# Performance work log

Hardware: AMD Instinct MI355X
Metric: run time of the kernel (lower is better)

## Reference

```python
import jax, jax.numpy as jnp
import numpy as np

N_NODES = 100000
N_EDGES = 3200000
F_IN = 512
HIDDEN = 64
N_CLASSES = 64


def setup_inputs() -> dict:
    key = jax.random.key(0)
    ks = jax.random.split(key, 6)
    node_features = jax.random.normal(ks[0], (N_NODES, F_IN), dtype=jnp.float32)
    edge_rows = jax.random.randint(ks[1], (N_EDGES,), 0, N_NODES, dtype=jnp.int32)
    edge_cols = jax.random.randint(ks[2], (N_EDGES,), 0, N_NODES, dtype=jnp.int32)
    edge_vals = jax.random.uniform(ks[3], (N_EDGES,), dtype=jnp.float32)
    W1 = jax.random.normal(ks[4], (F_IN, HIDDEN), dtype=jnp.float32) / np.sqrt(F_IN)
    b1 = jnp.zeros((HIDDEN,), dtype=jnp.float32)
    W2 = jax.random.normal(ks[5], (HIDDEN, N_CLASSES), dtype=jnp.float32) / np.sqrt(HIDDEN)
    b2 = jnp.zeros((N_CLASSES,), dtype=jnp.float32)
    return {
        "node_features": node_features,
        "edge_rows": edge_rows,
        "edge_cols": edge_cols,
        "edge_vals": edge_vals,
        "W1": W1,
        "b1": b1,
        "W2": W2,
        "b2": b2,
    }


def reference(node_features, edge_rows, edge_cols, edge_vals, W1, b1, W2, b2):
    # MLP node transform (inference: dropout is identity, no norms)
    h = jax.nn.relu(node_features @ W1 + b1)          # [N, HIDDEN]
    logits = h @ W2 + b2                              # [N, C]
    # smoother @ logits : sparse [N,N] COO times dense [N,C]
    messages = edge_vals[:, None] * logits[edge_cols]  # [E, C]
    out = jax.ops.segment_sum(messages, edge_rows, num_segments=N_NODES)
    return out
```

## Files before the change

### kernel.cpp

```cpp
#include <hip/hip_runtime.h>
#include <hip/hip_bf16.h>
#include <stdint.h>

#define N_NODES 100000
#define N_EDGES 3200000
#define F_IN    512
#define HIDDEN  64
#define NCLS    64

#define BROWS   64
#define NBKT    1563
#define CHUNK   4096
#define CAP     2432
#define NCOARSE 25
#define CAP1    135168
#define C2BLKS  33
#define OVF_CAP 8192
#define SENTINEL ((int)0x80000000)
#define NZERO   (NBKT*16 + NCOARSE*16 + 16)

typedef float v4f __attribute__((ext_vector_type(4)));
typedef short v8s __attribute__((ext_vector_type(8)));

__device__ __forceinline__ unsigned short f2bf(float f){
  unsigned u = __float_as_uint(f);
  u += 0x7fffu + ((u >> 16) & 1u);
  return (unsigned short)(u >> 16);
}
__device__ __forceinline__ float bflo(unsigned u){ return __uint_as_float(u << 16); }
__device__ __forceinline__ float bfhi(unsigned u){ return __uint_as_float(u & 0xffff0000u); }

__global__ void prep_weights(const float* __restrict__ W1, const float* __restrict__ W2,
                             unsigned short* __restrict__ w1f, unsigned short* __restrict__ w2f,
                             int* __restrict__ zeroc){
  int t = blockIdx.x * 256 + threadIdx.x;
  if (t < NZERO) zeroc[t] = 0;
  if (t < 16*4*64*8){
    int j = t & 7, lane = (t >> 3) & 63, nt = (t >> 9) & 3, ks = t >> 11;
    int m = lane & 15, q = lane >> 4;
    int k = ks*32 + q*8 + j, n = nt*16 + m;
    w1f[t] = f2bf(W1[k*HIDDEN + n]);
  } else {
    int u = t - 16*4*64*8;
    if (u < 2*4*64*8){
      int j = u & 7, lane = (u >> 3) & 63, nt = (u >> 9) & 3, ks = u >> 11;
      int m = lane & 15, q = lane >> 4;
      int k = ks*32 + q*8 + j, n = nt*16 + m;
      w2f[u] = f2bf(W2[k*NCLS + n]);
    }
  }
}

__global__ __launch_bounds__(256) void mlp_kernel(
    const float* __restrict__ X, const float* __restrict__ b1,
    const float* __restrict__ b2,
    const unsigned short* __restrict__ w1f, const unsigned short* __restrict__ w2f,
    unsigned short* __restrict__ logits){
  __shared__ __align__(16) float lds[4][16][68];
  int tid  = threadIdx.x;
  int wid  = tid >> 6, lane = tid & 63;
  int m    = lane & 15, q = lane >> 4;
  int base = blockIdx.x * 64 + wid * 16;
  if (base > N_NODES - 16) base = N_NODES - 16;

  const float* rp = X + (size_t)(base + m) * F_IN + q * 8;
  const v8s* w1v = (const v8s*)w1f;
  const v8s* w2v = (const v8s*)w2f;

  v4f a0c = {0,0,0,0}, a1c = {0,0,0,0}, a2c = {0,0,0,0}, a3c = {0,0,0,0};
  #pragma unroll
  for (int ks = 0; ks < 16; ++ks){
    const float4* pa = (const float4*)(rp + ks * 32);
    float4 x0 = pa[0], x1 = pa[1];
    v8s af;
    af[0]=(short)f2bf(x0.x); af[1]=(short)f2bf(x0.y); af[2]=(short)f2bf(x0.z); af[3]=(short)f2bf(x0.w);
    af[4]=(short)f2bf(x1.x); af[5]=(short)f2bf(x1.y); af[6]=(short)f2bf(x1.z); af[7]=(short)f2bf(x1.w);
    a0c = __builtin_amdgcn_mfma_f32_16x16x32_bf16(af, w1v[(ks*4+0)*64 + lane], a0c, 0,0,0);
    a1c = __builtin_amdgcn_mfma_f32_16x16x32_bf16(af, w1v[(ks*4+1)*64 + lane], a1c, 0,0,0);
    a2c = __builtin_amdgcn_mfma_f32_16x16x32_bf16(af, w1v[(ks*4+2)*64 + lane], a2c, 0,0,0);
    a3c = __builtin_amdgcn_mfma_f32_16x16x32_bf16(af, w1v[(ks*4+3)*64 + lane], a3c, 0,0,0);
  }

  float b1v0 = b1[m], b1v1 = b1[16+m], b1v2 = b1[32+m], b1v3 = b1[48+m];
  #pragma unroll
  for (int r = 0; r < 4; ++r){
    int row = q*4 + r;
    lds[wid][row][     m] = fmaxf(a0c[r] + b1v0, 0.f);
    lds[wid][row][16 + m] = fmaxf(a1c[r] + b1v1, 0.f);
    lds[wid][row][32 + m] = fmaxf(a2c[r] + b1v2, 0.f);
    lds[wid][row][48 + m] = fmaxf(a3c[r] + b1v3, 0.f);
  }
  __syncthreads();

  v4f c0 = {0,0,0,0}, c1 = {0,0,0,0}, c2 = {0,0,0,0}, c3 = {0,0,0,0};
  #pragma unroll
  for (int k2 = 0; k2 < 2; ++k2){
    const float4* ph = (const float4*)&lds[wid][m][k2*32 + q*8];
    float4 h0 = ph[0], h1 = ph[1];
    v8s af;
    af[0]=(short)f2bf(h0.x); af[1]=(short)f2bf(h0.y); af[2]=(short)f2bf(h0.z); af[3]=(short)f2bf(h0.w);
    af[4]=(short)f2bf(h1.x); af[5]=(short)f2bf(h1.y); af[6]=(short)f2bf(h1.z); af[7]=(short)f2bf(h1.w);
    c0 = __builtin_amdgcn_mfma_f32_16x16x32_bf16(af, w2v[(k2*4+0)*64 + lane], c0, 0,0,0);
    c1 = __builtin_amdgcn_mfma_f32_16x16x32_bf16(af, w2v[(k2*4+1)*64 + lane], c1, 0,0,0);
    c2 = __builtin_amdgcn_mfma_f32_16x16x32_bf16(af, w2v[(k2*4+2)*64 + lane], c2, 0,0,0);
    c3 = __builtin_amdgcn_mfma_f32_16x16x32_bf16(af, w2v[(k2*4+3)*64 + lane], c3, 0,0,0);
  }

  float b2v0 = b2[m], b2v1 = b2[16+m], b2v2 = b2[32+m], b2v3 = b2[48+m];
  unsigned short* lp = logits + (size_t)base * NCLS;
  #pragma unroll
  for (int r = 0; r < 4; ++r){
    int row = q*4 + r;
    lp[row*NCLS +      m] = f2bf(c0[r] + b2v0);
    lp[row*NCLS + 16 + m] = f2bf(c1[r] + b2v1);
    lp[row*NCLS + 32 + m] = f2bf(c2[r] + b2v2);
    lp[row*NCLS + 48 + m] = f2bf(c3[r] + b2v3);
  }
}

__global__ __launch_bounds__(256) void scat1(
    const int* __restrict__ rows, const int* __restrict__ cols,
    const float* __restrict__ vals, int* __restrict__ c1cur,
    int* __restrict__ ovf_cnt, int4* __restrict__ ovf,
    int2* __restrict__ ebkt1){
  __shared__ int  lcnt[32];
  __shared__ int  lbase[32];
  __shared__ int2 stage[CHUNK];
  __shared__ int  sdst[CHUNK];
  int t = threadIdx.x;
  int base = blockIdx.x * CHUNK;
  int cnt  = min(CHUNK, N_EDGES - base);

  if (t < 32) lcnt[t] = 0;
  __syncthreads();

  int r[16];
  #pragma unroll
  for (int k = 0; k < 16; ++k){
    int li = t + k*256;
    if (li < cnt){
      r[k] = rows[base + li];
      atomicAdd(&lcnt[r[k] >> 12], 1);
    } else r[k] = -1;
  }
  __syncthreads();

  if (t < 32){
    int cme = lcnt[t];
    int v = cme;
    #pragma unroll
    for (int o = 1; o < 32; o <<= 1){
      int u = __shfl_up(v, o);
      if (t >= o) v += u;
    }
    int excl = v - cme;
    if (cme){
      int g = atomicAdd(&c1cur[t*16], cme);
      lbase[t] = t*CAP1 + g - excl;
    }
    lcnt[t] = excl;
  }
  __syncthreads();

  #pragma unroll
  for (int k = 0; k < 16; ++k){
    if (r[k] >= 0){
      int li = t + k*256;
      int c  = cols[base + li];
      float vv = vals[base + li];
      int b  = r[k] >> 12;
      int pos = atomicAdd(&lcnt[b], 1);
      int dest = lbase[b] + pos;
      if (dest < b*CAP1 + CAP1){
        stage[pos] = make_int2(((r[k] & 4095) << 17) | c, __float_as_int(vv));
        sdst[pos]  = lbase[b];
      } else {
        sdst[pos] = SENTINEL;
        int o = atomicAdd(ovf_cnt, 1);
        if (o < OVF_CAP) ovf[o] = make_int4(r[k], c, __float_as_int(vv), 0);
      }
    }
  }
  __syncthreads();

  for (int j = t; j < cnt; j += 256){
    int d = sdst[j];
    if (d != SENTINEL) ebkt1[d + j] = stage[j];
  }
}

__global__ __launch_bounds__(256) void scat2(
    const int* __restrict__ c1cur, const int2* __restrict__ ebkt1,
    int* __restrict__ bcur, int* __restrict__ ovf_cnt, int4* __restrict__ ovf,
    int2* __restrict__ ebkt){
  __shared__ int  lcnt[64];
  __shared__ int  lbase[64];
  __shared__ int2 stage[CHUNK];
  __shared__ int  sdst[CHUNK];
  int t = threadIdx.x;
  int c = blockIdx.x / C2BLKS;
  int k0 = blockIdx.x % C2BLKS;

  int cntc = c1cur[c*16];
  if (cntc > CAP1) cntc = CAP1;
  int start = k0 * CHUNK;
  if (start >= cntc) return;
  int cnt = min(CHUNK, cntc - start);
  const int2* src = ebkt1 + (size_t)c * CAP1 + start;

  if (t < 64) lcnt[t] = 0;
  __syncthreads();

  int2 ev[16];
  #pragma unroll
  for (int k = 0; k < 16; ++k){
    int li = t + k*256;
    if (li < cnt){
      ev[k] = src[li];
      atomicAdd(&lcnt[(((unsigned)ev[k].x) >> 17) >> 6], 1);
    } else ev[k].x = -1;
  }
  __syncthreads();

  if (t < 64){
    int cme = lcnt[t];
    int v = cme;
    #pragma unroll
    for (int o = 1; o < 64; o <<= 1){
      int u = __shfl_up(v, o);
      if (t >= o) v += u;
    }
    int excl = v - cme;
    if (cme){
      int gb = c*64 + t;
      int g = atomicAdd(&bcur[gb*16], cme);
      lbase[t] = gb*CAP + g - excl;
    }
    lcnt[t] = excl;
  }
  __syncthreads();

  #pragma unroll
  for (int k = 0; k < 16; ++k){
    if (ev[k].x >= 0){
      unsigned x = (unsigned)ev[k].x;
      int lr12 = (int)(x >> 17);
      int fb   = lr12 >> 6;
      int pos = atomicAdd(&lcnt[fb], 1);
      int dest = lbase[fb] + pos;
      if (dest < (c*64 + fb)*CAP + CAP){
        stage[pos] = make_int2(((lr12 & 63) << 17) | (int)(x & 0x1FFFFu), ev[k].y);
        sdst[pos]  = lbase[fb];
      } else {
        sdst[pos] = SENTINEL;
        int o = atomicAdd(ovf_cnt, 1);
        if (o < OVF_CAP) ovf[o] = make_int4(c*4096 + lr12, (int)(x & 0x1FFFFu), ev[k].y, 0);
      }
    }
  }
  __syncthreads();

  for (int j = t; j < cnt; j += 256){
    int d = sdst[j];
    if (d != SENTINEL) ebkt[d + j] = stage[j];
  }
}

__global__ __launch_bounds__(256) void bucket_agg(
    const int* __restrict__ bcur, const int2* __restrict__ ebkt,
    const unsigned short* __restrict__ logits, float* __restrict__ out){
  __shared__ int2 sorted[CAP];
  __shared__ int  rc[BROWS];
  __shared__ int  rbase[BROWS + 1];
  __shared__ int  rcur[BROWS];
  int b = blockIdx.x, t = threadIdx.x;
  int w = t >> 6, lane = t & 63;
  int h = lane & 15, sel = lane >> 4;

  if (t < BROWS) rc[t] = 0;
  __syncthreads();

  int cnt = bcur[b * 16];
  if (cnt > CAP) cnt = CAP;
  const int2* ep = ebkt + (size_t)b * CAP;

  for (int j = t; j < cnt; j += 256){
    int x = ((const int*)ep)[2*j];
    atomicAdd(&rc[((unsigned)x) >> 17], 1);
  }
  __syncthreads();

  if (t < BROWS){
    int c = rc[t];
    int v = c;
    #pragma unroll
    for (int o = 1; o < 64; o <<= 1){
      int u = __shfl_up(v, o);
      if (lane >= o) v += u;
    }
    rbase[t + 1] = v;
    rcur[t]      = v - c;
    if (t == 0) rbase[0] = 0;
  }
  __syncthreads();

  for (int j = t; j < cnt; j += 256){
    int2 ev = ep[j];
    int pos = atomicAdd(&rcur[((unsigned)ev.x) >> 17], 1);
    sorted[pos] = ev;
  }
  __syncthreads();

  const uint2* lg = (const uint2*)logits;
  int row0 = b * BROWS;
  for (int n = w; n < BROWS; n += 4){
    int node = row0 + n;
    if (node >= N_NODES) break;
    int s = rbase[n], e = rbase[n + 1];
    float a0 = 0.f, a1 = 0.f, a2 = 0.f, a3 = 0.f;
    int i = s;
    for (; i + 16 <= e; i += 16){
      int2 e0 = sorted[i      + sel];
      int2 e1 = sorted[i + 4  + sel];
      int2 e2 = sorted[i + 8  + sel];
      int2 e3 = sorted[i + 12 + sel];
      uint2 u0 = lg[((size_t)(e0.x & 0x1FFFF) << 4) + h];
      uint2 u1 = lg[((size_t)(e1.x & 0x1FFFF) << 4) + h];
      uint2 u2 = lg[((size_t)(e2.x & 0x1FFFF) << 4) + h];
      uint2 u3 = lg[((size_t)(e3.x & 0x1FFFF) << 4) + h];
      float v0 = __int_as_float(e0.y), v1 = __int_as_float(e1.y);
      float v2 = __int_as_float(e2.y), v3 = __int_as_float(e3.y);
      a0 = fmaf(v0, bflo(u0.x), a0); a1 = fmaf(v0, bfhi(u0.x), a1);
      a2 = fmaf(v0, bflo(u0.y), a2); a3 = fmaf(v0, bfhi(u0.y), a3);
      a0 = fmaf(v1, bflo(u1.x), a0); a1 = fmaf(v1, bfhi(u1.x), a1);
      a2 = fmaf(v1, bflo(u1.y), a2); a3 = fmaf(v1, bfhi(u1.y), a3);
      a0 = fmaf(v2, bflo(u2.x), a0); a1 = fmaf(v2, bfhi(u2.x), a1);
      a2 = fmaf(v2, bflo(u2.y), a2); a3 = fmaf(v2, bfhi(u2.y), a3);
      a0 = fmaf(v3, bflo(u3.x), a0); a1 = fmaf(v3, bfhi(u3.x), a1);
      a2 = fmaf(v3, bflo(u3.y), a2); a3 = fmaf(v3, bfhi(u3.y), a3);
    }
    for (; i < e; i += 4){
      int idx = i + sel;
      int col = 0; float v = 0.f;
      if (idx < e){ int2 evv = sorted[idx]; col = evv.x & 0x1FFFF; v = __int_as_float(evv.y); }
      uint2 u = lg[((size_t)col << 4) + h];
      a0 = fmaf(v, bflo(u.x), a0); a1 = fmaf(v, bfhi(u.x), a1);
      a2 = fmaf(v, bflo(u.y), a2); a3 = fmaf(v, bfhi(u.y), a3);
    }
    a0 += __shfl_xor(a0, 16); a0 += __shfl_xor(a0, 32);
    a1 += __shfl_xor(a1, 16); a1 += __shfl_xor(a1, 32);
    a2 += __shfl_xor(a2, 16); a2 += __shfl_xor(a2, 32);
    a3 += __shfl_xor(a3, 16); a3 += __shfl_xor(a3, 32);
    if (sel == 0){
      float4* op = (float4*)(out + (size_t)node * NCLS);
      op[h] = make_float4(a0, a1, a2, a3);
    }
  }
}

__global__ __launch_bounds__(256) void ovf_apply(
    const int* __restrict__ ovf_cnt, const int4* __restrict__ ovf,
    const unsigned short* __restrict__ logits, float* __restrict__ out){
  int cnt = ovf_cnt[0];
  if (cnt > OVF_CAP) cnt = OVF_CAP;
  long total = (long)cnt * 64;
  for (long i = (long)blockIdx.x * 256 + threadIdx.x; i < total; i += (long)gridDim.x * 256){
    int e = (int)(i >> 6), c = (int)(i & 63);
    int4 ev = ovf[e];
    float lv = bflo(logits[((size_t)ev.y << 6) + c]);
    atomicAdd(&out[((size_t)ev.x << 6) + c], __int_as_float(ev.z) * lv);
  }
}

__global__ void scatter_atomic(const int* __restrict__ rows, const int* __restrict__ cols,
                               const float* __restrict__ vals,
                               const unsigned short* __restrict__ logits,
                               float* __restrict__ out){
  long g = (long)blockIdx.x * 256 + threadIdx.x;
  int e = (int)(g >> 6), c = (int)(g & 63);
  if (e < N_EDGES){
    float lv = __uint_as_float(((unsigned)logits[(size_t)cols[e] * NCLS + c]) << 16);
    atomicAdd(&out[(size_t)rows[e] * NCLS + c], vals[e] * lv);
  }
}

extern "C" void kernel_launch(void* const* d_in, const int* in_sizes, int n_in,
                              void* d_out, int out_size, void* d_ws, size_t ws_size,
                              hipStream_t stream){
  const float* X     = (const float*)d_in[0];
  const int*   erows = (const int*)  d_in[1];
  const int*   ecols = (const int*)  d_in[2];
  const float* evals = (const float*)d_in[3];
  const float* W1    = (const float*)d_in[4];
  const float* b1    = (const float*)d_in[5];
  const float* W2    = (const float*)d_in[6];
  const float* b2    = (const float*)d_in[7];
  float* out = (float*)d_out;

  char* ws = (char*)d_ws;
  size_t off = 0;
  auto alloc = [&](size_t bytes) -> char* {
    char* p = ws + off;
    off = (off + bytes + 255) & ~(size_t)255;
    return p;
  };
  unsigned short* logits = (unsigned short*)alloc((size_t)N_NODES * NCLS * 2);
  unsigned short* w1f    = (unsigned short*)alloc(16*4*64*8 * 2);
  unsigned short* w2f    = (unsigned short*)alloc(2*4*64*8 * 2);
  int*  bcur  = (int*)alloc((size_t)NZERO * 4);
  int*  c1cur = bcur + NBKT*16;
  int*  ovfc  = bcur + NBKT*16 + NCOARSE*16;
  int4* ovf   = (int4*)alloc((size_t)OVF_CAP * 16);
  int2* ebkt1 = (int2*)alloc((size_t)NCOARSE * CAP1 * 8);
  int2* ebkt  = (int2*)alloc((size_t)NBKT * CAP * 8);
  size_t full_need = off;

  prep_weights<<<144, 256, 0, stream>>>(W1, W2, w1f, w2f, bcur);
  mlp_kernel<<<(N_NODES + 63) / 64, 256, 0, stream>>>(X, b1, b2, w1f, w2f, logits);

  if (ws_size >= full_need){
    scat1<<<(N_EDGES + CHUNK - 1) / CHUNK, 256, 0, stream>>>(
        erows, ecols, evals, c1cur, ovfc, ovf, ebkt1);
    scat2<<<NCOARSE * C2BLKS, 256, 0, stream>>>(
        c1cur, ebkt1, bcur, ovfc, ovf, ebkt);
    bucket_agg<<<NBKT, 256, 0, stream>>>(bcur, ebkt, logits, out);
    ovf_apply<<<256, 256, 0, stream>>>(ovfc, ovf, logits, out);
  } else {
    hipMemsetAsync(out, 0, (size_t)N_NODES * NCLS * 4, stream);
    scatter_atomic<<<(int)(((long)N_EDGES * 64 + 255) / 256), 256, 0, stream>>>(
        erows, ecols, evals, logits, out);
  }
}
```

Baseline: 451.0 us.

## Co-schedule weight prep with edge scatter and MLP with second scatter pass

```diff
diff --git a/kernel.cpp b/kernel.cpp
--- a/kernel.cpp
+++ b/kernel.cpp
@@ -11,13 +11,19 @@
 #define BROWS   64
 #define NBKT    1563
 #define CHUNK   4096
+#define CHUNK2  2048
 #define CAP     2432
 #define NCOARSE 25
 #define CAP1    135168
-#define C2BLKS  33
+#define C2BLKS  66
 #define OVF_CAP 8192
 #define SENTINEL ((int)0x80000000)
 #define NZERO   (NBKT*16 + NCOARSE*16 + 16)
+
+#define PREP_BLKS 144
+#define SC1_BLKS  782
+#define MLP_BLKS  1563
+#define SC2_BLKS  (NCOARSE * C2BLKS)
 
 typedef float v4f __attribute__((ext_vector_type(4)));
 typedef short v8s __attribute__((ext_vector_type(8)));
@@ -30,105 +36,39 @@
 __device__ __forceinline__ float bflo(unsigned u){ return __uint_as_float(u << 16); }
 __device__ __forceinline__ float bfhi(unsigned u){ return __uint_as_float(u & 0xffff0000u); }
 
-__global__ void prep_weights(const float* __restrict__ W1, const float* __restrict__ W2,
-                             unsigned short* __restrict__ w1f, unsigned short* __restrict__ w2f,
-                             int* __restrict__ zeroc){
-  int t = blockIdx.x * 256 + threadIdx.x;
-  if (t < NZERO) zeroc[t] = 0;
-  if (t < 16*4*64*8){
-    int j = t & 7, lane = (t >> 3) & 63, nt = (t >> 9) & 3, ks = t >> 11;
-    int m = lane & 15, q = lane >> 4;
-    int k = ks*32 + q*8 + j, n = nt*16 + m;
-    w1f[t] = f2bf(W1[k*HIDDEN + n]);
-  } else {
-    int u = t - 16*4*64*8;
-    if (u < 2*4*64*8){
-      int j = u & 7, lane = (u >> 3) & 63, nt = (u >> 9) & 3, ks = u >> 11;
-      int m = lane & 15, q = lane >> 4;
-      int k = ks*32 + q*8 + j, n = nt*16 + m;
-      w2f[u] = f2bf(W2[k*NCLS + n]);
-    }
-  }
-}
-
-__global__ __launch_bounds__(256) void mlp_kernel(
-    const float* __restrict__ X, const float* __restrict__ b1,
-    const float* __restrict__ b2,
-    const unsigned short* __restrict__ w1f, const unsigned short* __restrict__ w2f,
-    unsigned short* __restrict__ logits){
-  __shared__ __align__(16) float lds[4][16][68];
-  int tid  = threadIdx.x;
-  int wid  = tid >> 6, lane = tid & 63;
-  int m    = lane & 15, q = lane >> 4;
-  int base = blockIdx.x * 64 + wid * 16;
-  if (base > N_NODES - 16) base = N_NODES - 16;
-
-  const float* rp = X + (size_t)(base + m) * F_IN + q * 8;
-  const v8s* w1v = (const v8s*)w1f;
-  const v8s* w2v = (const v8s*)w2f;
-
-  v4f a0c = {0,0,0,0}, a1c = {0,0,0,0}, a2c = {0,0,0,0}, a3c = {0,0,0,0};
-  #pragma unroll
-  for (int ks = 0; ks < 16; ++ks){
-    const float4* pa = (const float4*)(rp + ks * 32);
-    float4 x0 = pa[0], x1 = pa[1];
-    v8s af;
-    af[0]=(short)f2bf(x0.x); af[1]=(short)f2bf(x0.y); af[2]=(short)f2bf(x0.z); af[3]=(short)f2bf(x0.w);
-    af[4]=(short)f2bf(x1.x); af[5]=(short)f2bf(x1.y); af[6]=(short)f2bf(x1.z); af[7]=(short)f2bf(x1.w);
-    a0c = __builtin_amdgcn_mfma_f32_16x16x32_bf16(af, w1v[(ks*4+0)*64 + lane], a0c, 0,0,0);
-    a1c = __builtin_amdgcn_mfma_f32_16x16x32_bf16(af, w1v[(ks*4+1)*64 + lane], a1c, 0,0,0);
-    a2c = __builtin_amdgcn_mfma_f32_16x16x32_bf16(af, w1v[(ks*4+2)*64 + lane], a2c, 0,0,0);
-    a3c = __builtin_amdgcn_mfma_f32_16x16x32_bf16(af, w1v[(ks*4+3)*64 + lane], a3c, 0,0,0);
-  }
-
-  float b1v0 = b1[m], b1v1 = b1[16+m], b1v2 = b1[32+m], b1v3 = b1[48+m];
-  #pragma unroll
-  for (int r = 0; r < 4; ++r){
-    int row = q*4 + r;
-    lds[wid][row][     m] = fmaxf(a0c[r] + b1v0, 0.f);
-    lds[wid][row][16 + m] = fmaxf(a1c[r] + b1v1, 0.f);
-    lds[wid][row][32 + m] = fmaxf(a2c[r] + b1v2, 0.f);
-    lds[wid][row][48 + m] = fmaxf(a3c[r] + b1v3, 0.f);
-  }
-  __syncthreads();
-
-  v4f c0 = {0,0,0,0}, c1 = {0,0,0,0}, c2 = {0,0,0,0}, c3 = {0,0,0,0};
-  #pragma unroll
-  for (int k2 = 0; k2 < 2; ++k2){
-    const float4* ph = (const float4*)&lds[wid][m][k2*32 + q*8];
-    float4 h0 = ph[0], h1 = ph[1];
-    v8s af;
-    af[0]=(short)f2bf(h0.x); af[1]=(short)f2bf(h0.y); af[2]=(short)f2bf(h0.z); af[3]=(short)f2bf(h0.w);
-    af[4]=(short)f2bf(h1.x); af[5]=(short)f2bf(h1.y); af[6]=(short)f2bf(h1.z); af[7]=(short)f2bf(h1.w);
-    c0 = __builtin_amdgcn_mfma_f32_16x16x32_bf16(af, w2v[(k2*4+0)*64 + lane], c0, 0,0,0);
-    c1 = __builtin_amdgcn_mfma_f32_16x16x32_bf16(af, w2v[(k2*4+1)*64 + lane], c1, 0,0,0);
-    c2 = __builtin_amdgcn_mfma_f32_16x16x32_bf16(af, w2v[(k2*4+2)*64 + lane], c2, 0,0,0);
-    c3 = __builtin_amdgcn_mfma_f32_16x16x32_bf16(af, w2v[(k2*4+3)*64 + lane], c3, 0,0,0);
-  }
-
-  float b2v0 = b2[m], b2v1 = b2[16+m], b2v2 = b2[32+m], b2v3 = b2[48+m];
-  unsigned short* lp = logits + (size_t)base * NCLS;
-  #pragma unroll
-  for (int r = 0; r < 4; ++r){
-    int row = q*4 + r;
-    lp[row*NCLS +      m] = f2bf(c0[r] + b2v0);
-    lp[row*NCLS + 16 + m] = f2bf(c1[r] + b2v1);
-    lp[row*NCLS + 32 + m] = f2bf(c2[r] + b2v2);
-    lp[row*NCLS + 48 + m] = f2bf(c3[r] + b2v3);
-  }
-}
-
-__global__ __launch_bounds__(256) void scat1(
+__global__ __launch_bounds__(256) void k1(
     const int* __restrict__ rows, const int* __restrict__ cols,
     const float* __restrict__ vals, int* __restrict__ c1cur,
     int* __restrict__ ovf_cnt, int4* __restrict__ ovf,
-    int2* __restrict__ ebkt1){
+    int2* __restrict__ ebkt1,
+    const float* __restrict__ W1, const float* __restrict__ W2,
+    unsigned short* __restrict__ w1f, unsigned short* __restrict__ w2f){
   __shared__ int  lcnt[32];
   __shared__ int  lbase[32];
   __shared__ int2 stage[CHUNK];
   __shared__ int  sdst[CHUNK];
   int t = threadIdx.x;
-  int base = blockIdx.x * CHUNK;
+
+  if (blockIdx.x < PREP_BLKS){
+    int g = blockIdx.x * 256 + t;
+    if (g < 16*4*64*8){
+      int j = g & 7, lane = (g >> 3) & 63, nt = (g >> 9) & 3, ks = g >> 11;
+      int m = lane & 15, q = lane >> 4;
+      int k = ks*32 + q*8 + j, n = nt*16 + m;
+      w1f[g] = f2bf(W1[k*HIDDEN + n]);
+    } else {
+      int u = g - 16*4*64*8;
+      if (u < 2*4*64*8){
+        int j = u & 7, lane = (u >> 3) & 63, nt = (u >> 9) & 3, ks = u >> 11;
+        int m = lane & 15, q = lane >> 4;
+        int k = ks*32 + q*8 + j, n = nt*16 + m;
+        w2f[u] = f2bf(W2[k*NCLS + n]);
+      }
+    }
+    return;
+  }
+
+  int base = (blockIdx.x - PREP_BLKS) * CHUNK;
   int cnt  = min(CHUNK, N_EDGES - base);
 
   if (t < 32) lcnt[t] = 0;
@@ -189,32 +129,102 @@
   }
 }
 
-__global__ __launch_bounds__(256) void scat2(
+__global__ __launch_bounds__(256) void k2(
+    const float* __restrict__ X, const float* __restrict__ b1,
+    const float* __restrict__ b2,
+    const unsigned short* __restrict__ w1f, const unsigned short* __restrict__ w2f,
+    unsigned short* __restrict__ logits,
     const int* __restrict__ c1cur, const int2* __restrict__ ebkt1,
     int* __restrict__ bcur, int* __restrict__ ovf_cnt, int4* __restrict__ ovf,
     int2* __restrict__ ebkt){
-  __shared__ int  lcnt[64];
-  __shared__ int  lbase[64];
-  __shared__ int2 stage[CHUNK];
-  __shared__ int  sdst[CHUNK];
-  int t = threadIdx.x;
-  int c = blockIdx.x / C2BLKS;
-  int k0 = blockIdx.x % C2BLKS;
+  __shared__ __align__(16) char smem[25088];
+  int tid = threadIdx.x;
+
+  if (blockIdx.x < MLP_BLKS){
+    float (*lds)[16][68] = (float (*)[16][68])smem;
+    int wid  = tid >> 6, lane = tid & 63;
+    int m    = lane & 15, q = lane >> 4;
+    int base = blockIdx.x * 64 + wid * 16;
+    if (base > N_NODES - 16) base = N_NODES - 16;
+
+    const float* rp = X + (size_t)(base + m) * F_IN + q * 8;
+    const v8s* w1v = (const v8s*)w1f;
+    const v8s* w2v = (const v8s*)w2f;
+
+    v4f a0c = {0,0,0,0}, a1c = {0,0,0,0}, a2c = {0,0,0,0}, a3c = {0,0,0,0};
+    #pragma unroll
+    for (int ks = 0; ks < 16; ++ks){
+      const float4* pa = (const float4*)(rp + ks * 32);
+      float4 x0 = pa[0], x1 = pa[1];
+      v8s af;
+      af[0]=(short)f2bf(x0.x); af[1]=(short)f2bf(x0.y); af[2]=(short)f2bf(x0.z); af[3]=(short)f2bf(x0.w);
+      af[4]=(short)f2bf(x1.x); af[5]=(short)f2bf(x1.y); af[6]=(short)f2bf(x1.z); af[7]=(short)f2bf(x1.w);
+      a0c = __builtin_amdgcn_mfma_f32_16x16x32_bf16(af, w1v[(ks*4+0)*64 + lane], a0c, 0,0,0);
+      a1c = __builtin_amdgcn_mfma_f32_16x16x32_bf16(af, w1v[(ks*4+1)*64 + lane], a1c, 0,0,0);
+      a2c = __builtin_amdgcn_mfma_f32_16x16x32_bf16(af, w1v[(ks*4+2)*64 + lane], a2c, 0,0,0);
+      a3c = __builtin_amdgcn_mfma_f32_16x16x32_bf16(af, w1v[(ks*4+3)*64 + lane], a3c, 0,0,0);
+    }
+
+    float b1v0 = b1[m], b1v1 = b1[16+m], b1v2 = b1[32+m], b1v3 = b1[48+m];
+    #pragma unroll
+    for (int r = 0; r < 4; ++r){
+      int row = q*4 + r;
+      lds[wid][row][     m] = fmaxf(a0c[r] + b1v0, 0.f);
+      lds[wid][row][16 + m] = fmaxf(a1c[r] + b1v1, 0.f);
+      lds[wid][row][32 + m] = fmaxf(a2c[r] + b1v2, 0.f);
+      lds[wid][row][48 + m] = fmaxf(a3c[r] + b1v3, 0.f);
+    }
+    __syncthreads();
+
+    v4f c0 = {0,0,0,0}, c1 = {0,0,0,0}, c2 = {0,0,0,0}, c3 = {0,0,0,0};
+    #pragma unroll
+    for (int k2i = 0; k2i < 2; ++k2i){
+      const float4* ph = (const float4*)&lds[wid][m][k2i*32 + q*8];
+      float4 h0 = ph[0], h1 = ph[1];
+      v8s af;
+      af[0]=(short)f2bf(h0.x); af[1]=(short)f2bf(h0.y); af[2]=(short)f2bf(h0.z); af[3]=(short)f2bf(h0.w);
+      af[4]=(short)f2bf(h1.x); af[5]=(short)f2bf(h1.y); af[6]=(short)f2bf(h1.z); af[7]=(short)f2bf(h1.w);
+      c0 = __builtin_amdgcn_mfma_f32_16x16x32_bf16(af, w2v[(k2i*4+0)*64 + lane], c0, 0,0,0);
+      c1 = __builtin_amdgcn_mfma_f32_16x16x32_bf16(af, w2v[(k2i*4+1)*64 + lane], c1, 0,0,0);
+      c2 = __builtin_amdgcn_mfma_f32_16x16x32_bf16(af, w2v[(k2i*4+2)*64 + lane], c2, 0,0,0);
+      c3 = __builtin_amdgcn_mfma_f32_16x16x32_bf16(af, w2v[(k2i*4+3)*64 + lane], c3, 0,0,0);
+    }
+
+    float b2v0 = b2[m], b2v1 = b2[16+m], b2v2 = b2[32+m], b2v3 = b2[48+m];
+    unsigned short* lp = logits + (size_t)base * NCLS;
+    #pragma unroll
+    for (int r = 0; r < 4; ++r){
+      int row = q*4 + r;
+      lp[row*NCLS +      m] = f2bf(c0[r] + b2v0);
+      lp[row*NCLS + 16 + m] = f2bf(c1[r] + b2v1);
+      lp[row*NCLS + 32 + m] = f2bf(c2[r] + b2v2);
+      lp[row*NCLS + 48 + m] = f2bf(c3[r] + b2v3);
+    }
+    return;
+  }
+
+  int2* stage = (int2*)smem;
+  int*  sdst  = (int*)(smem + 16384);
+  int*  lcnt  = (int*)(smem + 24576);
+  int*  lbase = (int*)(smem + 24832);
+  int sbid = blockIdx.x - MLP_BLKS;
+  int c  = sbid / C2BLKS;
+  int k0 = sbid % C2BLKS;
 
   int cntc = c1cur[c*16];
   if (cntc > CAP1) cntc = CAP1;
-  int start = k0 * CHUNK;
+  int start = k0 * CHUNK2;
   if (start >= cntc) return;
-  int cnt = min(CHUNK, cntc - start);
+  int cnt = min(CHUNK2, cntc - start);
   const int2* src = ebkt1 + (size_t)c * CAP1 + start;
 
-  if (t < 64) lcnt[t] = 0;
-  __syncthreads();
-
-  int2 ev[16];
+  if (tid < 64) lcnt[tid] = 0;
+  __syncthreads();
+
+  int2 ev[8];
   #pragma unroll
-  for (int k = 0; k < 16; ++k){
-    int li = t + k*256;
+  for (int k = 0; k < 8; ++k){
+    int li = tid + k*256;
     if (li < cnt){
       ev[k] = src[li];
       atomicAdd(&lcnt[(((unsigned)ev[k].x) >> 17) >> 6], 1);
@@ -222,26 +232,26 @@
   }
   __syncthreads();
 
-  if (t < 64){
-    int cme = lcnt[t];
+  if (tid < 64){
+    int cme = lcnt[tid];
     int v = cme;
     #pragma unroll
     for (int o = 1; o < 64; o <<= 1){
       int u = __shfl_up(v, o);
-      if (t >= o) v += u;
+      if (tid >= o) v += u;
     }
     int excl = v - cme;
     if (cme){
-      int gb = c*64 + t;
+      int gb = c*64 + tid;
       int g = atomicAdd(&bcur[gb*16], cme);
-      lbase[t] = gb*CAP + g - excl;
-    }
-    lcnt[t] = excl;
+      lbase[tid] = gb*CAP + g - excl;
+    }
+    lcnt[tid] = excl;
   }
   __syncthreads();
 
   #pragma unroll
-  for (int k = 0; k < 16; ++k){
+  for (int k = 0; k < 8; ++k){
     if (ev[k].x >= 0){
       unsigned x = (unsigned)ev[k].x;
       int lr12 = (int)(x >> 17);
@@ -260,7 +270,7 @@
   }
   __syncthreads();
 
-  for (int j = t; j < cnt; j += 256){
+  for (int j = tid; j < cnt; j += 256){
     int d = sdst[j];
     if (d != SENTINEL) ebkt[d + j] = stage[j];
   }
@@ -268,7 +278,8 @@
 
 __global__ __launch_bounds__(256) void bucket_agg(
     const int* __restrict__ bcur, const int2* __restrict__ ebkt,
-    const unsigned short* __restrict__ logits, float* __restrict__ out){
+    const unsigned short* __restrict__ logits, float* __restrict__ out,
+    const int* __restrict__ ovf_cnt, const int4* __restrict__ ovfl){
   __shared__ int2 sorted[CAP];
   __shared__ int  rc[BROWS];
   __shared__ int  rbase[BROWS + 1];
@@ -283,6 +294,8 @@
   int cnt = bcur[b * 16];
   if (cnt > CAP) cnt = CAP;
   const int2* ep = ebkt + (size_t)b * CAP;
+  int ocnt = ovf_cnt[0];
+  if (ocnt > OVF_CAP) ocnt = OVF_CAP;
 
   for (int j = t; j < cnt; j += 256){
     int x = ((const int*)ep)[2*j];
@@ -352,23 +365,20 @@
     a2 += __shfl_xor(a2, 16); a2 += __shfl_xor(a2, 32);
     a3 += __shfl_xor(a3, 16); a3 += __shfl_xor(a3, 32);
     if (sel == 0){
+      if (ocnt){
+        for (int j = 0; j < ocnt; ++j){
+          int4 eo = ovfl[j];
+          if (eo.x == node){
+            uint2 u = lg[((size_t)eo.y << 4) + h];
+            float v = __int_as_float(eo.z);
+            a0 = fmaf(v, bflo(u.x), a0); a1 = fmaf(v, bfhi(u.x), a1);
+            a2 = fmaf(v, bflo(u.y), a2); a3 = fmaf(v, bfhi(u.y), a3);
+          }
+        }
+      }
       float4* op = (float4*)(out + (size_t)node * NCLS);
       op[h] = make_float4(a0, a1, a2, a3);
     }
-  }
-}
-
-__global__ __launch_bounds__(256) void ovf_apply(
-    const int* __restrict__ ovf_cnt, const int4* __restrict__ ovf,
-    const unsigned short* __restrict__ logits, float* __restrict__ out){
-  int cnt = ovf_cnt[0];
-  if (cnt > OVF_CAP) cnt = OVF_CAP;
-  long total = (long)cnt * 64;
-  for (long i = (long)blockIdx.x * 256 + threadIdx.x; i < total; i += (long)gridDim.x * 256){
-    int e = (int)(i >> 6), c = (int)(i & 63);
-    int4 ev = ovf[e];
-    float lv = bflo(logits[((size_t)ev.y << 6) + c]);
-    atomicAdd(&out[((size_t)ev.x << 6) + c], __int_as_float(ev.z) * lv);
   }
 }
 
@@ -415,17 +425,18 @@
   int2* ebkt  = (int2*)alloc((size_t)NBKT * CAP * 8);
   size_t full_need = off;
 
-  prep_weights<<<144, 256, 0, stream>>>(W1, W2, w1f, w2f, bcur);
-  mlp_kernel<<<(N_NODES + 63) / 64, 256, 0, stream>>>(X, b1, b2, w1f, w2f, logits);
-
   if (ws_size >= full_need){
-    scat1<<<(N_EDGES + CHUNK - 1) / CHUNK, 256, 0, stream>>>(
-        erows, ecols, evals, c1cur, ovfc, ovf, ebkt1);
-    scat2<<<NCOARSE * C2BLKS, 256, 0, stream>>>(
-        c1cur, ebkt1, bcur, ovfc, ovf, ebkt);
-    bucket_agg<<<NBKT, 256, 0, stream>>>(bcur, ebkt, logits, out);
-    ovf_apply<<<256, 256, 0, stream>>>(ovfc, ovf, logits, out);
+    hipMemsetAsync(bcur, 0, (size_t)NZERO * 4, stream);
+    k1<<<PREP_BLKS + SC1_BLKS, 256, 0, stream>>>(
+        erows, ecols, evals, c1cur, ovfc, ovf, ebkt1, W1, W2, w1f, w2f);
+    k2<<<MLP_BLKS + SC2_BLKS, 256, 0, stream>>>(
+        X, b1, b2, w1f, w2f, logits, c1cur, ebkt1, bcur, ovfc, ovf, ebkt);
+    bucket_agg<<<NBKT, 256, 0, stream>>>(bcur, ebkt, logits, out, ovfc, ovf);
   } else {
+    k1<<<PREP_BLKS, 256, 0, stream>>>(
+        erows, ecols, evals, c1cur, ovfc, ovf, ebkt1, W1, W2, w1f, w2f);
+    k2<<<MLP_BLKS, 256, 0, stream>>>(
+        X, b1, b2, w1f, w2f, logits, c1cur, ebkt1, bcur, ovfc, ovf, ebkt);
     hipMemsetAsync(out, 0, (size_t)N_NODES * NCLS * 4, stream);
     scatter_atomic<<<(int)(((long)N_EDGES * 64 + 255) / 256), 256, 0, stream>>>(
         erows, ecols, evals, logits, out);
```

Result: faster. 436.7 us (-3.2%).
